# Performance work log

Measured on AMD Instinct MI355X. Metric: run time of the kernel, lower is better.

The kernel has to match this reference:

```python
import jax, jax.numpy as jnp
import numpy as np
import math

D_MODEL = 1024
N_HEADS = 16
SLOT_DIM = 64
N_SLOTS = 1024
TOP_K = 2
LN_EPS = 1e-5


def setup_inputs() -> dict:
    key = jax.random.key(0)
    ks = jax.random.split(key, 8)
    x = jax.random.normal(ks[0], (4, 2048, D_MODEL), dtype=jnp.float32)
    ln_gamma = jnp.ones((D_MODEL,), jnp.float32)
    ln_beta = jnp.zeros((D_MODEL,), jnp.float32)
    q_w = jax.random.normal(ks[1], (N_HEADS * SLOT_DIM, D_MODEL), jnp.float32) / math.sqrt(D_MODEL)
    q_b = jnp.zeros((N_HEADS * SLOT_DIM,), jnp.float32)
    slot_signatures = jax.random.normal(ks[2], (N_HEADS, N_SLOTS, SLOT_DIM), jnp.float32) * 0.5
    slot_values = jax.random.normal(ks[3], (N_HEADS, N_SLOTS, SLOT_DIM), jnp.float32) * 0.02
    out_w = jax.random.normal(ks[4], (D_MODEL, N_HEADS * SLOT_DIM), jnp.float32) / math.sqrt(N_HEADS * SLOT_DIM)
    out_b = jnp.zeros((D_MODEL,), jnp.float32)
    temperature = jnp.ones((1,), jnp.float32)
    return {"x": x, "ln_gamma": ln_gamma, "ln_beta": ln_beta, "q_w": q_w, "q_b": q_b,
            "slot_signatures": slot_signatures, "slot_values": slot_values,
            "out_w": out_w, "out_b": out_b, "temperature": temperature}


def _ternary_ste(sig):
    # forward = {-1,0,+1} quantization; backward = identity (straight-through)
    q = jnp.where(sig > 0.3, 1.0, jnp.where(sig < -0.3, -1.0, 0.0))
    return sig + jax.lax.stop_gradient(q - sig)


def reference(x, ln_gamma, ln_beta, q_w, q_b, slot_signatures, slot_values, out_w, out_b, temperature):
    B, T, D = x.shape
    # LayerNorm
    mean = jnp.mean(x, axis=-1, keepdims=True)
    var = jnp.var(x, axis=-1, keepdims=True)
    x_norm = (x - mean) * jax.lax.rsqrt(var + LN_EPS) * ln_gamma + ln_beta
    # Query projection -> [B, T, H, slot_dim]
    q = (x_norm @ q_w.T + q_b).reshape(B, T, N_HEADS, SLOT_DIM)
    sigs = _ternary_ste(slot_signatures)  # [H, S, d]
    scores = jnp.einsum('bthd,hsd->bths', q, sigs)
    scores = scores / (temperature * math.sqrt(SLOT_DIM))  # [B, T, H, S]
    # top-k routing
    topk_scores, slot_idx = jax.lax.top_k(scores, TOP_K)  # [B, T, H, K]
    weights = jax.nn.softmax(topk_scores, axis=-1)
    # gather selected slot values: [B, T, H, K, d]
    h_idx = jnp.arange(N_HEADS)[None, None, :, None]
    selected = slot_values[h_idx, slot_idx]
    read = jnp.sum(selected * weights[..., None], axis=3)  # [B, T, H, d]
    read = read.reshape(B, T, N_HEADS * SLOT_DIM)
    out = read @ out_w.T + out_b
    return x + out
```

## Files before the change

### kernel.cpp

```cpp
#include <hip/hip_runtime.h>

typedef unsigned short u16;
typedef unsigned int   u32;
typedef float f32x4  __attribute__((ext_vector_type(4)));
typedef __bf16 bf16x8 __attribute__((ext_vector_type(8)));

__device__ __forceinline__ u16 f2bf(float f){
  u32 u = __float_as_uint(f);
  u += 0x7fffu + ((u >> 16) & 1u);
  return (u16)(u >> 16);
}

__device__ __forceinline__ void gld16(const void* g, void* l){
  __builtin_amdgcn_global_load_lds((const __attribute__((address_space(1))) u32*)g,
                                   (__attribute__((address_space(3))) u32*)l, 16, 0, 0);
}

__global__ __launch_bounds__(256) void convert_kernel(
    const float* __restrict__ qw, const float* __restrict__ ow,
    const float* __restrict__ sg,
    u16* __restrict__ qwb, u16* __restrict__ owb, u16* __restrict__ sgb){
  int i = (blockIdx.x * 256 + threadIdx.x) * 4;
  f32x4 a = *(const f32x4*)(qw + i);
  f32x4 b = *(const f32x4*)(ow + i);
  f32x4 s = *(const f32x4*)(sg + i);
  uint2 pa, pb, ps;
  pa.x = (u32)f2bf(a[0]) | ((u32)f2bf(a[1]) << 16);
  pa.y = (u32)f2bf(a[2]) | ((u32)f2bf(a[3]) << 16);
  pb.x = (u32)f2bf(b[0]) | ((u32)f2bf(b[1]) << 16);
  pb.y = (u32)f2bf(b[2]) | ((u32)f2bf(b[3]) << 16);
  float t0 = (s[0] > 0.3f) ? 1.0f : ((s[0] < -0.3f) ? -1.0f : 0.0f);
  float t1 = (s[1] > 0.3f) ? 1.0f : ((s[1] < -0.3f) ? -1.0f : 0.0f);
  float t2 = (s[2] > 0.3f) ? 1.0f : ((s[2] < -0.3f) ? -1.0f : 0.0f);
  float t3 = (s[3] > 0.3f) ? 1.0f : ((s[3] < -0.3f) ? -1.0f : 0.0f);
  ps.x = (u32)f2bf(t0) | ((u32)f2bf(t1) << 16);
  ps.y = (u32)f2bf(t2) | ((u32)f2bf(t3) << 16);
  *(uint2*)(qwb + i) = pa;
  *(uint2*)(owb + i) = pb;
  *(uint2*)(sgb + i) = ps;
}

__global__ __launch_bounds__(256) void ln_kernel(
    const float* __restrict__ x, const float* __restrict__ g,
    const float* __restrict__ b, u16* __restrict__ xn){
  const int tid = threadIdx.x, lane = tid & 63, w = tid >> 6;
  const int t = blockIdx.x * 4 + w;
  const float* xr = x + (size_t)t * 1024;
  f32x4 v[4];
  #pragma unroll
  for (int j = 0; j < 4; ++j) v[j] = *(const f32x4*)(xr + j * 256 + lane * 4);
  float s = 0.f, ss = 0.f;
  #pragma unroll
  for (int j = 0; j < 4; ++j)
    #pragma unroll
    for (int e = 0; e < 4; ++e){ s += v[j][e]; ss += v[j][e] * v[j][e]; }
  #pragma unroll
  for (int off = 32; off; off >>= 1){
    s  += __shfl_xor(s, off);
    ss += __shfl_xor(ss, off);
  }
  float mean = s * (1.0f / 1024.0f);
  float var  = ss * (1.0f / 1024.0f) - mean * mean;
  float rs   = rsqrtf(var + 1e-5f);
  #pragma unroll
  for (int j = 0; j < 4; ++j){
    f32x4 gv = *(const f32x4*)(g + j * 256 + lane * 4);
    f32x4 bv = *(const f32x4*)(b + j * 256 + lane * 4);
    float y0 = (v[j][0]-mean)*rs*gv[0]+bv[0];
    float y1 = (v[j][1]-mean)*rs*gv[1]+bv[1];
    float y2 = (v[j][2]-mean)*rs*gv[2]+bv[2];
    float y3 = (v[j][3]-mean)*rs*gv[3]+bv[3];
    uint2 pk;
    pk.x = (u32)f2bf(y0) | ((u32)f2bf(y1) << 16);
    pk.y = (u32)f2bf(y2) | ((u32)f2bf(y3) << 16);
    *(uint2*)(xn + (size_t)t * 1024 + j * 256 + lane * 4) = pk;
  }
}

__global__ __launch_bounds__(256, 2) void gemm_bt(
    const u16* __restrict__ A, const u16* __restrict__ B,
    const float* __restrict__ bias, const float* __restrict__ resid,
    float* __restrict__ outf, u16* __restrict__ outb, int mode){
  __shared__ u16 As[2][128 * 64];
  __shared__ u16 Bs[2][128 * 64];
  const int tid = threadIdx.x;
  const int b = blockIdx.x;
  const int m0 = ((b & 7) * 8 + ((b >> 3) & 7)) * 128;
  const int n0 = (b >> 6) * 128;
  const int w = tid >> 6, lane = tid & 63, lm = lane & 15, quad = lane >> 4;
  const int wm = (w & 1) * 64, wn = (w >> 1) * 64;
  const int lr = lane >> 3;
  const int lg = (lane & 7) ^ lr;
  const f32x4 fz = {0.f, 0.f, 0.f, 0.f};
  f32x4 acc[4][4];
  #pragma unroll
  for (int i = 0; i < 4; ++i)
    #pragma unroll
    for (int j = 0; j < 4; ++j) acc[i][j] = fz;

  const u16* gA = A + (size_t)(m0 + w * 32 + lr) * 1024 + lg * 8;
  const u16* gB = B + (size_t)(n0 + w * 32 + lr) * 1024 + lg * 8;
  const int lbase = (w * 32) * 64;
  const int sw = lm & 7;

  auto stage = [&](int kt, int bb){
    #pragma unroll
    for (int sub = 0; sub < 4; ++sub){
      gld16(gA + (size_t)(sub * 8) * 1024 + kt * 64, &As[bb][lbase + sub * 8 * 64]);
      gld16(gB + (size_t)(sub * 8) * 1024 + kt * 64, &Bs[bb][lbase + sub * 8 * 64]);
    }
  };

  stage(0, 0);
  for (int kt = 0; kt < 16; ++kt){
    __syncthreads();
    if (kt < 15) stage(kt + 1, (kt + 1) & 1);
    const u16* as = As[kt & 1];
    const u16* bs = Bs[kt & 1];
    #pragma unroll
    for (int kk = 0; kk < 2; ++kk){
      const int ch = ((quad + kk * 4) ^ sw) * 8;
      bf16x8 afr[4], bfr[4];
      #pragma unroll
      for (int i = 0; i < 4; ++i)
        afr[i] = *(const bf16x8*)(&as[(wm + i * 16 + lm) * 64 + ch]);
      #pragma unroll
      for (int j = 0; j < 4; ++j)
        bfr[j] = *(const bf16x8*)(&bs[(wn + j * 16 + lm) * 64 + ch]);
      #pragma unroll
      for (int i = 0; i < 4; ++i)
        #pragma unroll
        for (int j = 0; j < 4; ++j)
          acc[i][j] = __builtin_amdgcn_mfma_f32_16x16x32_bf16(afr[i], bfr[j], acc[i][j], 0, 0, 0);
    }
  }

  #pragma unroll
  for (int i = 0; i < 4; ++i){
    #pragma unroll
    for (int r = 0; r < 4; ++r){
      int grow = m0 + wm + i * 16 + quad * 4 + r;
      #pragma unroll
      for (int j = 0; j < 4; ++j){
        int gcol = n0 + wn + j * 16 + lm;
        float v = acc[i][j][r] + bias[gcol];
        if (mode){
          v += resid[(size_t)grow * 1024 + gcol];
          outf[(size_t)grow * 1024 + gcol] = v;
        } else {
          outb[(size_t)grow * 1024 + gcol] = f2bf(v);
        }
      }
    }
  }
}

__global__ __launch_bounds__(256) void route3_kernel(
    const u16* __restrict__ q, const u16* __restrict__ sig,
    const float* __restrict__ V, const float* __restrict__ temp,
    u16* __restrict__ rd){
  const int h = blockIdx.y;
  const int tid = threadIdx.x, w = tid >> 6, lane = tid & 63;
  const int lm = lane & 15, quad = lane >> 4;
  const int t0 = blockIdx.x * 256 + w * 64;

  bf16x8 qf[4][2];
  #pragma unroll
  for (int s = 0; s < 4; ++s){
    const u16* qp = q + (size_t)(t0 + s * 16 + lm) * 1024 + h * 64 + quad * 8;
    qf[s][0] = *(const bf16x8*)(qp);
    qf[s][1] = *(const bf16x8*)(qp + 32);
  }

  const u16* sp = sig + (size_t)h * 65536 + lm * 64 + quad * 8;
  bf16x8 c0 = *(const bf16x8*)(sp);
  bf16x8 c1 = *(const bf16x8*)(sp + 32);
  bf16x8 n0 = *(const bf16x8*)(sp + 1024);
  bf16x8 n1 = *(const bf16x8*)(sp + 1024 + 32);
  sp += 2048;

  const f32x4 fz = {0.f, 0.f, 0.f, 0.f};
  const u32 MASK = 0xFFFFFC00u;
  float v1[4], v2[4];
  #pragma unroll
  for (int s = 0; s < 4; ++s){ v1[s] = -3.0e38f; v2[s] = -3.0e38f; }
  u32 rk0 = (u32)(quad * 4), rk1 = rk0 + 1, rk2 = rk0 + 2, rk3 = rk0 + 3;

  for (int t = 0; t < 64; ++t){
    #pragma unroll
    for (int s = 0; s < 4; ++s){
      f32x4 acc = __builtin_amdgcn_mfma_f32_16x16x32_bf16(c0, qf[s][0], fz, 0, 0, 0);
      acc       = __builtin_amdgcn_mfma_f32_16x16x32_bf16(c1, qf[s][1], acc, 0, 0, 0);
      float k0 = __uint_as_float((__float_as_uint(acc[0]) & MASK) | rk0);
      float k1 = __uint_as_float((__float_as_uint(acc[1]) & MASK) | rk1);
      float k2 = __uint_as_float((__float_as_uint(acc[2]) & MASK) | rk2);
      float k3 = __uint_as_float((__float_as_uint(acc[3]) & MASK) | rk3);
      float o;
      o = v1[s]; v1[s] = fmaxf(o, k0); v2[s] = __builtin_amdgcn_fmed3f(o, v2[s], k0);
      o = v1[s]; v1[s] = fmaxf(o, k1); v2[s] = __builtin_amdgcn_fmed3f(o, v2[s], k1);
      o = v1[s]; v1[s] = fmaxf(o, k2); v2[s] = __builtin_amdgcn_fmed3f(o, v2[s], k2);
      o = v1[s]; v1[s] = fmaxf(o, k3); v2[s] = __builtin_amdgcn_fmed3f(o, v2[s], k3);
    }
    c0 = n0; c1 = n1;
    if (t < 62){
      n0 = *(const bf16x8*)(sp);
      n1 = *(const bf16x8*)(sp + 32);
      sp += 1024;
    }
    rk0 += 16u; rk1 += 16u; rk2 += 16u; rk3 += 16u;
  }

  #pragma unroll
  for (int off = 16; off <= 32; off <<= 1){
    #pragma unroll
    for (int s = 0; s < 4; ++s){
      float o1 = __shfl_xor(v1[s], off);
      float o2 = __shfl_xor(v2[s], off);
      float ov = v1[s];
      v1[s] = fmaxf(ov, o1);
      v2[s] = __builtin_amdgcn_fmed3f(ov, o1, fmaxf(v2[s], o2));
    }
  }

  float a1 = (quad & 1) ? v1[1] : v1[0], b1 = (quad & 1) ? v1[3] : v1[2];
  float a2 = (quad & 1) ? v2[1] : v2[0], b2 = (quad & 1) ? v2[3] : v2[2];
  float V1 = (quad & 2) ? b1 : a1;
  float V2 = (quad & 2) ? b2 : a2;
  u32 u1 = __float_as_uint(V1), u2 = __float_as_uint(V2);
  int I1 = (int)(u1 & 1023u), I2 = (int)(u2 & 1023u);
  float s1 = __uint_as_float(u1 & MASK);
  float s2 = __uint_as_float(u2 & MASK);
  float tsc = 1.0f / (temp[0] * 8.0f);
  float ex = __expf((s2 - s1) * tsc);
  float iw = 1.0f / (1.0f + ex);
  float W1 = iw, W2 = ex * iw;

  const float* va = V + ((size_t)h * 1024 + I1) * 64;
  const float* vb = V + ((size_t)h * 1024 + I2) * 64;
  u16* dst = rd + (size_t)(t0 + lane) * 1024 + h * 64;
  #pragma unroll
  for (int g = 0; g < 4; ++g){
    f32x4 xa = *(const f32x4*)(va + g * 16);
    f32x4 xb = *(const f32x4*)(va + g * 16 + 4);
    f32x4 xc = *(const f32x4*)(va + g * 16 + 8);
    f32x4 xd = *(const f32x4*)(va + g * 16 + 12);
    f32x4 ya = *(const f32x4*)(vb + g * 16);
    f32x4 yb = *(const f32x4*)(vb + g * 16 + 4);
    f32x4 yc = *(const f32x4*)(vb + g * 16 + 8);
    f32x4 yd = *(const f32x4*)(vb + g * 16 + 12);
    uint4 o;
    o.x = (u32)f2bf(W1*xa[0]+W2*ya[0]) | ((u32)f2bf(W1*xa[1]+W2*ya[1]) << 16);
    o.y = (u32)f2bf(W1*xa[2]+W2*ya[2]) | ((u32)f2bf(W1*xa[3]+W2*ya[3]) << 16);
    o.z = (u32)f2bf(W1*xb[0]+W2*yb[0]) | ((u32)f2bf(W1*xb[1]+W2*yb[1]) << 16);
    o.w = (u32)f2bf(W1*xb[2]+W2*yb[2]) | ((u32)f2bf(W1*xb[3]+W2*yb[3]) << 16);
    uint4 p;
    p.x = (u32)f2bf(W1*xc[0]+W2*yc[0]) | ((u32)f2bf(W1*xc[1]+W2*yc[1]) << 16);
    p.y = (u32)f2bf(W1*xc[2]+W2*yc[2]) | ((u32)f2bf(W1*xc[3]+W2*yc[3]) << 16);
    p.z = (u32)f2bf(W1*xd[0]+W2*yd[0]) | ((u32)f2bf(W1*xd[1]+W2*yd[1]) << 16);
    p.w = (u32)f2bf(W1*xd[2]+W2*yd[2]) | ((u32)f2bf(W1*xd[3]+W2*yd[3]) << 16);
    *(uint4*)(dst + g * 16) = o;
    *(uint4*)(dst + g * 16 + 8) = p;
  }
}

extern "C" void kernel_launch(void* const* d_in, const int* in_sizes, int n_in,
                              void* d_out, int out_size, void* d_ws, size_t ws_size,
                              hipStream_t stream){
  const float* x    = (const float*)d_in[0];
  const float* lng  = (const float*)d_in[1];
  const float* lnb  = (const float*)d_in[2];
  const float* qw   = (const float*)d_in[3];
  const float* qb   = (const float*)d_in[4];
  const float* sig  = (const float*)d_in[5];
  const float* sv   = (const float*)d_in[6];
  const float* ow   = (const float*)d_in[7];
  const float* ob   = (const float*)d_in[8];
  const float* temp = (const float*)d_in[9];
  float* out = (float*)d_out;

  char* ws = (char*)d_ws;
  u16* xn   = (u16*)(ws);
  u16* qwb  = (u16*)(ws + 16777216);
  u16* owb  = (u16*)(ws + 16777216 + 2097152);
  u16* sgb  = (u16*)(ws + 16777216 + 2 * 2097152);
  u16* qb16 = (u16*)(ws + 16777216 + 3 * 2097152);
  u16* rdb  = xn;

  convert_kernel<<<1024, 256, 0, stream>>>(qw, ow, sig, qwb, owb, sgb);
  ln_kernel<<<2048, 256, 0, stream>>>(x, lng, lnb, xn);
  gemm_bt<<<512, 256, 0, stream>>>(xn, qwb, qb, nullptr, nullptr, qb16, 0);
  route3_kernel<<<dim3(32, 16), 256, 0, stream>>>(qb16, sgb, sv, temp, rdb);
  gemm_bt<<<512, 256, 0, stream>>>(rdb, owb, ob, x, out, nullptr, 1);
}
```

Measured before the change: 216.3 us.

## Split slot scan across wave pairs and merge convert with layernorm kernel

The routing kernel now splits the 1024 slots between two waves per token group and merges their top-2 candidates through shared memory, doubling the grid to 64x16 blocks. Each wave runs half as many serial MFMA/top-2 iterations, which shortens the critical path and raises occupancy. The gather phase is split so two threads share each token's 64-wide output. Separately, the weight-convert and layernorm kernels are fused into one launch to save one kernel launch gap. The cost is an extra __syncthreads plus a shared-memory merge, and each query fragment is loaded twice.

```diff
diff --git a/kernel.cpp b/kernel.cpp
--- a/kernel.cpp
+++ b/kernel.cpp
@@ -16,64 +16,65 @@
                                    (__attribute__((address_space(3))) u32*)l, 16, 0, 0);
 }
 
-__global__ __launch_bounds__(256) void convert_kernel(
-    const float* __restrict__ qw, const float* __restrict__ ow,
-    const float* __restrict__ sg,
-    u16* __restrict__ qwb, u16* __restrict__ owb, u16* __restrict__ sgb){
-  int i = (blockIdx.x * 256 + threadIdx.x) * 4;
-  f32x4 a = *(const f32x4*)(qw + i);
-  f32x4 b = *(const f32x4*)(ow + i);
-  f32x4 s = *(const f32x4*)(sg + i);
-  uint2 pa, pb, ps;
-  pa.x = (u32)f2bf(a[0]) | ((u32)f2bf(a[1]) << 16);
-  pa.y = (u32)f2bf(a[2]) | ((u32)f2bf(a[3]) << 16);
-  pb.x = (u32)f2bf(b[0]) | ((u32)f2bf(b[1]) << 16);
-  pb.y = (u32)f2bf(b[2]) | ((u32)f2bf(b[3]) << 16);
-  float t0 = (s[0] > 0.3f) ? 1.0f : ((s[0] < -0.3f) ? -1.0f : 0.0f);
-  float t1 = (s[1] > 0.3f) ? 1.0f : ((s[1] < -0.3f) ? -1.0f : 0.0f);
-  float t2 = (s[2] > 0.3f) ? 1.0f : ((s[2] < -0.3f) ? -1.0f : 0.0f);
-  float t3 = (s[3] > 0.3f) ? 1.0f : ((s[3] < -0.3f) ? -1.0f : 0.0f);
-  ps.x = (u32)f2bf(t0) | ((u32)f2bf(t1) << 16);
-  ps.y = (u32)f2bf(t2) | ((u32)f2bf(t3) << 16);
-  *(uint2*)(qwb + i) = pa;
-  *(uint2*)(owb + i) = pb;
-  *(uint2*)(sgb + i) = ps;
-}
-
-__global__ __launch_bounds__(256) void ln_kernel(
-    const float* __restrict__ x, const float* __restrict__ g,
-    const float* __restrict__ b, u16* __restrict__ xn){
-  const int tid = threadIdx.x, lane = tid & 63, w = tid >> 6;
-  const int t = blockIdx.x * 4 + w;
-  const float* xr = x + (size_t)t * 1024;
-  f32x4 v[4];
-  #pragma unroll
-  for (int j = 0; j < 4; ++j) v[j] = *(const f32x4*)(xr + j * 256 + lane * 4);
-  float s = 0.f, ss = 0.f;
-  #pragma unroll
-  for (int j = 0; j < 4; ++j)
-    #pragma unroll
-    for (int e = 0; e < 4; ++e){ s += v[j][e]; ss += v[j][e] * v[j][e]; }
-  #pragma unroll
-  for (int off = 32; off; off >>= 1){
-    s  += __shfl_xor(s, off);
-    ss += __shfl_xor(ss, off);
-  }
-  float mean = s * (1.0f / 1024.0f);
-  float var  = ss * (1.0f / 1024.0f) - mean * mean;
-  float rs   = rsqrtf(var + 1e-5f);
-  #pragma unroll
-  for (int j = 0; j < 4; ++j){
-    f32x4 gv = *(const f32x4*)(g + j * 256 + lane * 4);
-    f32x4 bv = *(const f32x4*)(b + j * 256 + lane * 4);
-    float y0 = (v[j][0]-mean)*rs*gv[0]+bv[0];
-    float y1 = (v[j][1]-mean)*rs*gv[1]+bv[1];
-    float y2 = (v[j][2]-mean)*rs*gv[2]+bv[2];
-    float y3 = (v[j][3]-mean)*rs*gv[3]+bv[3];
-    uint2 pk;
-    pk.x = (u32)f2bf(y0) | ((u32)f2bf(y1) << 16);
-    pk.y = (u32)f2bf(y2) | ((u32)f2bf(y3) << 16);
-    *(uint2*)(xn + (size_t)t * 1024 + j * 256 + lane * 4) = pk;
+__global__ __launch_bounds__(256) void prep_kernel(
+    const float* __restrict__ x, const float* __restrict__ lng,
+    const float* __restrict__ lnb, const float* __restrict__ qw,
+    const float* __restrict__ ow, const float* __restrict__ sg,
+    u16* __restrict__ xn, u16* __restrict__ qwb,
+    u16* __restrict__ owb, u16* __restrict__ sgb){
+  const int b = blockIdx.x, tid = threadIdx.x;
+  if (b < 1024){
+    int i = (b * 256 + tid) * 4;
+    f32x4 a = *(const f32x4*)(qw + i);
+    f32x4 c = *(const f32x4*)(ow + i);
+    f32x4 s = *(const f32x4*)(sg + i);
+    uint2 pa, pb, ps;
+    pa.x = (u32)f2bf(a[0]) | ((u32)f2bf(a[1]) << 16);
+    pa.y = (u32)f2bf(a[2]) | ((u32)f2bf(a[3]) << 16);
+    pb.x = (u32)f2bf(c[0]) | ((u32)f2bf(c[1]) << 16);
+    pb.y = (u32)f2bf(c[2]) | ((u32)f2bf(c[3]) << 16);
+    float t0 = (s[0] > 0.3f) ? 1.0f : ((s[0] < -0.3f) ? -1.0f : 0.0f);
+    float t1 = (s[1] > 0.3f) ? 1.0f : ((s[1] < -0.3f) ? -1.0f : 0.0f);
+    float t2 = (s[2] > 0.3f) ? 1.0f : ((s[2] < -0.3f) ? -1.0f : 0.0f);
+    float t3 = (s[3] > 0.3f) ? 1.0f : ((s[3] < -0.3f) ? -1.0f : 0.0f);
+    ps.x = (u32)f2bf(t0) | ((u32)f2bf(t1) << 16);
+    ps.y = (u32)f2bf(t2) | ((u32)f2bf(t3) << 16);
+    *(uint2*)(qwb + i) = pa;
+    *(uint2*)(owb + i) = pb;
+    *(uint2*)(sgb + i) = ps;
+  } else {
+    const int lane = tid & 63, w = tid >> 6;
+    const int t = (b - 1024) * 4 + w;
+    const float* xr = x + (size_t)t * 1024;
+    f32x4 v[4];
+    #pragma unroll
+    for (int j = 0; j < 4; ++j) v[j] = *(const f32x4*)(xr + j * 256 + lane * 4);
+    float s = 0.f, ss = 0.f;
+    #pragma unroll
+    for (int j = 0; j < 4; ++j)
+      #pragma unroll
+      for (int e = 0; e < 4; ++e){ s += v[j][e]; ss += v[j][e] * v[j][e]; }
+    #pragma unroll
+    for (int off = 32; off; off >>= 1){
+      s  += __shfl_xor(s, off);
+      ss += __shfl_xor(ss, off);
+    }
+    float mean = s * (1.0f / 1024.0f);
+    float var  = ss * (1.0f / 1024.0f) - mean * mean;
+    float rs   = rsqrtf(var + 1e-5f);
+    #pragma unroll
+    for (int j = 0; j < 4; ++j){
+      f32x4 gv = *(const f32x4*)(lng + j * 256 + lane * 4);
+      f32x4 bv = *(const f32x4*)(lnb + j * 256 + lane * 4);
+      float y0 = (v[j][0]-mean)*rs*gv[0]+bv[0];
+      float y1 = (v[j][1]-mean)*rs*gv[1]+bv[1];
+      float y2 = (v[j][2]-mean)*rs*gv[2]+bv[2];
+      float y3 = (v[j][3]-mean)*rs*gv[3]+bv[3];
+      uint2 pk;
+      pk.x = (u32)f2bf(y0) | ((u32)f2bf(y1) << 16);
+      pk.y = (u32)f2bf(y2) | ((u32)f2bf(y3) << 16);
+      *(uint2*)(xn + (size_t)t * 1024 + j * 256 + lane * 4) = pk;
+    }
   }
 }
 
@@ -162,17 +163,20 @@
   const int h = blockIdx.y;
   const int tid = threadIdx.x, w = tid >> 6, lane = tid & 63;
   const int lm = lane & 15, quad = lane >> 4;
-  const int t0 = blockIdx.x * 256 + w * 64;
+  const int s = w & 1, g = w >> 1;
+  const int t0 = blockIdx.x * 128 + g * 64;
+
+  __shared__ float sv[2][2][64][2];
 
   bf16x8 qf[4][2];
   #pragma unroll
-  for (int s = 0; s < 4; ++s){
-    const u16* qp = q + (size_t)(t0 + s * 16 + lm) * 1024 + h * 64 + quad * 8;
-    qf[s][0] = *(const bf16x8*)(qp);
-    qf[s][1] = *(const bf16x8*)(qp + 32);
-  }
-
-  const u16* sp = sig + (size_t)h * 65536 + lm * 64 + quad * 8;
+  for (int st = 0; st < 4; ++st){
+    const u16* qp = q + (size_t)(t0 + st * 16 + lm) * 1024 + h * 64 + quad * 8;
+    qf[st][0] = *(const bf16x8*)(qp);
+    qf[st][1] = *(const bf16x8*)(qp + 32);
+  }
+
+  const u16* sp = sig + (size_t)h * 65536 + (size_t)(s * 512 + lm) * 64 + quad * 8;
   bf16x8 c0 = *(const bf16x8*)(sp);
   bf16x8 c1 = *(const bf16x8*)(sp + 32);
   bf16x8 n0 = *(const bf16x8*)(sp + 1024);
@@ -183,26 +187,26 @@
   const u32 MASK = 0xFFFFFC00u;
   float v1[4], v2[4];
   #pragma unroll
-  for (int s = 0; s < 4; ++s){ v1[s] = -3.0e38f; v2[s] = -3.0e38f; }
-  u32 rk0 = (u32)(quad * 4), rk1 = rk0 + 1, rk2 = rk0 + 2, rk3 = rk0 + 3;
-
-  for (int t = 0; t < 64; ++t){
-    #pragma unroll
-    for (int s = 0; s < 4; ++s){
-      f32x4 acc = __builtin_amdgcn_mfma_f32_16x16x32_bf16(c0, qf[s][0], fz, 0, 0, 0);
-      acc       = __builtin_amdgcn_mfma_f32_16x16x32_bf16(c1, qf[s][1], acc, 0, 0, 0);
+  for (int st = 0; st < 4; ++st){ v1[st] = -3.0e38f; v2[st] = -3.0e38f; }
+  u32 rk0 = (u32)(s * 512 + quad * 4), rk1 = rk0 + 1, rk2 = rk0 + 2, rk3 = rk0 + 3;
+
+  for (int t = 0; t < 32; ++t){
+    #pragma unroll
+    for (int st = 0; st < 4; ++st){
+      f32x4 acc = __builtin_amdgcn_mfma_f32_16x16x32_bf16(c0, qf[st][0], fz, 0, 0, 0);
+      acc       = __builtin_amdgcn_mfma_f32_16x16x32_bf16(c1, qf[st][1], acc, 0, 0, 0);
       float k0 = __uint_as_float((__float_as_uint(acc[0]) & MASK) | rk0);
       float k1 = __uint_as_float((__float_as_uint(acc[1]) & MASK) | rk1);
       float k2 = __uint_as_float((__float_as_uint(acc[2]) & MASK) | rk2);
       float k3 = __uint_as_float((__float_as_uint(acc[3]) & MASK) | rk3);
       float o;
-      o = v1[s]; v1[s] = fmaxf(o, k0); v2[s] = __builtin_amdgcn_fmed3f(o, v2[s], k0);
-      o = v1[s]; v1[s] = fmaxf(o, k1); v2[s] = __builtin_amdgcn_fmed3f(o, v2[s], k1);
-      o = v1[s]; v1[s] = fmaxf(o, k2); v2[s] = __builtin_amdgcn_fmed3f(o, v2[s], k2);
-      o = v1[s]; v1[s] = fmaxf(o, k3); v2[s] = __builtin_amdgcn_fmed3f(o, v2[s], k3);
+      o = v1[st]; v1[st] = fmaxf(o, k0); v2[st] = __builtin_amdgcn_fmed3f(o, v2[st], k0);
+      o = v1[st]; v1[st] = fmaxf(o, k1); v2[st] = __builtin_amdgcn_fmed3f(o, v2[st], k1);
+      o = v1[st]; v1[st] = fmaxf(o, k2); v2[st] = __builtin_amdgcn_fmed3f(o, v2[st], k2);
+      o = v1[st]; v1[st] = fmaxf(o, k3); v2[st] = __builtin_amdgcn_fmed3f(o, v2[st], k3);
     }
     c0 = n0; c1 = n1;
-    if (t < 62){
+    if (t < 30){
       n0 = *(const bf16x8*)(sp);
       n1 = *(const bf16x8*)(sp + 32);
       sp += 1024;
@@ -213,19 +217,29 @@
   #pragma unroll
   for (int off = 16; off <= 32; off <<= 1){
     #pragma unroll
-    for (int s = 0; s < 4; ++s){
-      float o1 = __shfl_xor(v1[s], off);
-      float o2 = __shfl_xor(v2[s], off);
-      float ov = v1[s];
-      v1[s] = fmaxf(ov, o1);
-      v2[s] = __builtin_amdgcn_fmed3f(ov, o1, fmaxf(v2[s], o2));
-    }
-  }
-
-  float a1 = (quad & 1) ? v1[1] : v1[0], b1 = (quad & 1) ? v1[3] : v1[2];
-  float a2 = (quad & 1) ? v2[1] : v2[0], b2 = (quad & 1) ? v2[3] : v2[2];
-  float V1 = (quad & 2) ? b1 : a1;
-  float V2 = (quad & 2) ? b2 : a2;
+    for (int st = 0; st < 4; ++st){
+      float o1 = __shfl_xor(v1[st], off);
+      float o2 = __shfl_xor(v2[st], off);
+      float ov = v1[st];
+      v1[st] = fmaxf(ov, o1);
+      v2[st] = __builtin_amdgcn_fmed3f(ov, o1, fmaxf(v2[st], o2));
+    }
+  }
+
+  {
+    float a1 = (quad & 1) ? v1[1] : v1[0], b1 = (quad & 1) ? v1[3] : v1[2];
+    float a2 = (quad & 1) ? v2[1] : v2[0], b2 = (quad & 1) ? v2[3] : v2[2];
+    sv[g][s][lane][0] = (quad & 2) ? b1 : a1;
+    sv[g][s][lane][1] = (quad & 2) ? b2 : a2;
+  }
+  __syncthreads();
+
+  const int tk = tid >> 1, hd = tid & 1;
+  const int gg = tk >> 6, ll = tk & 63;
+  float a1 = sv[gg][0][ll][0], a2 = sv[gg][0][ll][1];
+  float b1 = sv[gg][1][ll][0], b2 = sv[gg][1][ll][1];
+  float V1 = fmaxf(a1, b1);
+  float V2 = __builtin_amdgcn_fmed3f(a1, b1, fmaxf(a2, b2));
   u32 u1 = __float_as_uint(V1), u2 = __float_as_uint(V2);
   int I1 = (int)(u1 & 1023u), I2 = (int)(u2 & 1023u);
   float s1 = __uint_as_float(u1 & MASK);
@@ -235,19 +249,19 @@
   float iw = 1.0f / (1.0f + ex);
   float W1 = iw, W2 = ex * iw;
 
-  const float* va = V + ((size_t)h * 1024 + I1) * 64;
-  const float* vb = V + ((size_t)h * 1024 + I2) * 64;
-  u16* dst = rd + (size_t)(t0 + lane) * 1024 + h * 64;
-  #pragma unroll
-  for (int g = 0; g < 4; ++g){
-    f32x4 xa = *(const f32x4*)(va + g * 16);
-    f32x4 xb = *(const f32x4*)(va + g * 16 + 4);
-    f32x4 xc = *(const f32x4*)(va + g * 16 + 8);
-    f32x4 xd = *(const f32x4*)(va + g * 16 + 12);
-    f32x4 ya = *(const f32x4*)(vb + g * 16);
-    f32x4 yb = *(const f32x4*)(vb + g * 16 + 4);
-    f32x4 yc = *(const f32x4*)(vb + g * 16 + 8);
-    f32x4 yd = *(const f32x4*)(vb + g * 16 + 12);
+  const float* va = V + ((size_t)h * 1024 + I1) * 64 + hd * 32;
+  const float* vb = V + ((size_t)h * 1024 + I2) * 64 + hd * 32;
+  u16* dst = rd + (size_t)(blockIdx.x * 128 + tk) * 1024 + h * 64 + hd * 32;
+  #pragma unroll
+  for (int gr = 0; gr < 2; ++gr){
+    f32x4 xa = *(const f32x4*)(va + gr * 16);
+    f32x4 xb = *(const f32x4*)(va + gr * 16 + 4);
+    f32x4 xc = *(const f32x4*)(va + gr * 16 + 8);
+    f32x4 xd = *(const f32x4*)(va + gr * 16 + 12);
+    f32x4 ya = *(const f32x4*)(vb + gr * 16);
+    f32x4 yb = *(const f32x4*)(vb + gr * 16 + 4);
+    f32x4 yc = *(const f32x4*)(vb + gr * 16 + 8);
+    f32x4 yd = *(const f32x4*)(vb + gr * 16 + 12);
     uint4 o;
     o.x = (u32)f2bf(W1*xa[0]+W2*ya[0]) | ((u32)f2bf(W1*xa[1]+W2*ya[1]) << 16);
     o.y = (u32)f2bf(W1*xa[2]+W2*ya[2]) | ((u32)f2bf(W1*xa[3]+W2*ya[3]) << 16);
@@ -258,8 +272,8 @@
     p.y = (u32)f2bf(W1*xc[2]+W2*yc[2]) | ((u32)f2bf(W1*xc[3]+W2*yc[3]) << 16);
     p.z = (u32)f2bf(W1*xd[0]+W2*yd[0]) | ((u32)f2bf(W1*xd[1]+W2*yd[1]) << 16);
     p.w = (u32)f2bf(W1*xd[2]+W2*yd[2]) | ((u32)f2bf(W1*xd[3]+W2*yd[3]) << 16);
-    *(uint4*)(dst + g * 16) = o;
-    *(uint4*)(dst + g * 16 + 8) = p;
+    *(uint4*)(dst + gr * 16) = o;
+    *(uint4*)(dst + gr * 16 + 8) = p;
   }
 }
 
@@ -286,9 +300,8 @@
   u16* qb16 = (u16*)(ws + 16777216 + 3 * 2097152);
   u16* rdb  = xn;
 
-  convert_kernel<<<1024, 256, 0, stream>>>(qw, ow, sig, qwb, owb, sgb);
-  ln_kernel<<<2048, 256, 0, stream>>>(x, lng, lnb, xn);
+  prep_kernel<<<3072, 256, 0, stream>>>(x, lng, lnb, qw, ow, sig, xn, qwb, owb, sgb);
   gemm_bt<<<512, 256, 0, stream>>>(xn, qwb, qb, nullptr, nullptr, qb16, 0);
-  route3_kernel<<<dim3(32, 16), 256, 0, stream>>>(qb16, sgb, sv, temp, rdb);
+  route3_kernel<<<dim3(64, 16), 256, 0, stream>>>(qb16, sgb, sv, temp, rdb);
   gemm_bt<<<512, 256, 0, stream>>>(rdb, owb, ob, x, out, nullptr, 1);
 }
```

New measurement: 215.0 us. About the same (-0.6%).
